# Performance work log

Measured on AMD Instinct MI355X. Metric: run time of the kernel, lower is better.

The kernel has to match this reference:

```python
import jax, jax.numpy as jnp
import numpy as np

N, E, D, R = 50000, 800000, 128, 16
NUM_OBJS, NUM_ATTRS, L = 179, 10, 5
OBJ_DIM, ATTR_DIM, HID, NANGLE = 96, 32, 512, 24


def setup_inputs() -> dict:
    key = jax.random.key(0)
    ks = jax.random.split(key, 20)
    z = jax.random.normal(ks[0], (N, D), dtype=jnp.float32)
    objs = jax.random.randint(ks[1], (N,), 0, NUM_OBJS + 1)
    s = jax.random.randint(ks[2], (E,), 0, N)
    o = jax.random.randint(ks[3], (E,), 0, N)
    p = jax.random.randint(ks[4], (E,), 0, R)
    triples = jnp.stack([s, p, o], axis=1)
    attributes = jax.random.randint(ks[5], (N,), 0, NUM_ATTRS)
    w = 0.05
    obj_emb = jax.random.normal(ks[6], (NUM_OBJS + 1, OBJ_DIM), dtype=jnp.float32)
    attr_emb = jax.random.normal(ks[7], (NUM_ATTRS, ATTR_DIM), dtype=jnp.float32)
    Wrel = jax.random.normal(ks[8], (L, R, D, D), dtype=jnp.float32) * w
    Wroot = jax.random.normal(ks[9], (L, D, D), dtype=jnp.float32) * w
    bconv = jnp.zeros((L, D), dtype=jnp.float32)
    box_W1 = jax.random.normal(ks[10], (2 * D + ATTR_DIM, HID), dtype=jnp.float32) * w
    box_b1 = jnp.zeros((HID,), dtype=jnp.float32)
    box_W2 = jax.random.normal(ks[11], (HID, 6), dtype=jnp.float32) * w
    box_b2 = jnp.zeros((6,), dtype=jnp.float32)
    ang_W1 = jax.random.normal(ks[12], (2 * D, HID), dtype=jnp.float32) * w
    ang_b1 = jnp.zeros((HID,), dtype=jnp.float32)
    ang_W2 = jax.random.normal(ks[13], (HID, NANGLE), dtype=jnp.float32) * w
    ang_b2 = jnp.zeros((NANGLE,), dtype=jnp.float32)
    return dict(z=z, objs=objs, triples=triples, attributes=attributes,
                obj_emb=obj_emb, attr_emb=attr_emb, Wrel=Wrel, Wroot=Wroot,
                bconv=bconv, box_W1=box_W1, box_b1=box_b1, box_W2=box_W2,
                box_b2=box_b2, ang_W1=ang_W1, ang_b1=ang_b1, ang_W2=ang_W2,
                ang_b2=ang_b2)


def _rgcn_layer(x, s, o, p, Wr, Wroot_l, b):
    # relation-typed transform of all nodes: [N, R, D]
    h_rel = jnp.einsum('nd,rdf->nrf', x, Wr)
    msgs = h_rel[s, p]                                   # [E, D] gather
    # mean aggregation per (target, relation), as in PyG RGCNConv
    seg = o * R + p
    cnt = jax.ops.segment_sum(jnp.ones((s.shape[0],), x.dtype), seg,
                              num_segments=x.shape[0] * R)
    deg = jnp.maximum(cnt[seg], 1.0)
    agg = jax.ops.segment_sum(msgs / deg[:, None], o, num_segments=x.shape[0])
    return x @ Wroot_l + agg + b


def reference(z, objs, triples, attributes, obj_emb, attr_emb, Wrel, Wroot,
              bconv, box_W1, box_b1, box_W2, box_b2, ang_W1, ang_b1,
              ang_W2, ang_b2):
    s, p, o = triples[:, 0], triples[:, 1], triples[:, 2]
    attr_vecs = attr_emb[attributes]                     # [N, 32]
    obj_vecs = jnp.concatenate([obj_emb[objs], attr_vecs], axis=1)  # [N, 128]
    for j in range(L):
        obj_vecs = jax.nn.relu(_rgcn_layer(obj_vecs, s, o, p,
                                           Wrel[j], Wroot[j], bconv[j]))
    obj_vecs = jnp.concatenate([obj_vecs, z], axis=1)    # [N, 256]
    obj_vecs_box = jnp.concatenate([obj_vecs, attr_vecs], axis=1)  # [N, 288]
    boxes_pred = jax.nn.relu(obj_vecs_box @ box_W1 + box_b1) @ box_W2 + box_b2
    ang_h = jax.nn.relu(obj_vecs @ ang_W1 + ang_b1) @ ang_W2 + ang_b2
    angles_pred = jax.nn.log_softmax(ang_h, axis=1)
    return boxes_pred, angles_pred
```

## Files before the change

### kernel.cpp

```cpp
#include <hip/hip_runtime.h>
#include <hip/hip_bf16.h>
#include <math.h>

#define NN   50000
#define EE   800000
#define RREL 16
#define LLAY 5
#define NBINS (NN * RREL)
#define HCAP 565248

typedef __attribute__((ext_vector_type(8))) short s8v;
typedef __attribute__((ext_vector_type(4))) float f4v;

__device__ __forceinline__ unsigned short f2bf(float f) {
  __hip_bfloat16 h = __float2bfloat16(f);
  return __builtin_bit_cast(unsigned short, h);
}
__device__ __forceinline__ float bf2f(unsigned int u) {
  return __builtin_bit_cast(float, u << 16);
}
__device__ __forceinline__ void split1(float v, unsigned short& h, unsigned short& l) {
  __hip_bfloat16 hb = __float2bfloat16(v);
  float hf = __bfloat162float(hb);
  h = __builtin_bit_cast(unsigned short, hb);
  __hip_bfloat16 lb = __float2bfloat16(v - hf);
  l = __builtin_bit_cast(unsigned short, lb);
}

__global__ void build_x0_kernel(const int* __restrict__ objs, const int* __restrict__ attrs,
                                const float* __restrict__ obj_emb, const float* __restrict__ attr_emb,
                                unsigned short* __restrict__ xh) {
  int t = blockIdx.x * blockDim.x + threadIdx.x;
  if (t >= NN * 32) return;
  int n = t >> 5, q = t & 31;
  float4 v;
  if (q < 24) v = *(const float4*)&obj_emb[(size_t)objs[n] * 96 + q * 4];
  else        v = *(const float4*)&attr_emb[(size_t)attrs[n] * 32 + (q - 24) * 4];
  ushort4 h;
  h.x = f2bf(v.x); h.y = f2bf(v.y); h.z = f2bf(v.z); h.w = f2bf(v.w);
  *(ushort4*)&xh[(size_t)n * 128 + q * 4] = h;
}

__global__ void prep_zattr(const float* __restrict__ z, const int* __restrict__ attrs,
                           const float* __restrict__ attr_emb,
                           unsigned short* __restrict__ zh, unsigned short* __restrict__ ah) {
  int t = blockIdx.x * blockDim.x + threadIdx.x;
  if (t >= NN * 40) return;
  int n = t / 40, q = t % 40;
  float4 v;
  ushort4 h;
  if (q < 32) {
    v = *(const float4*)&z[(size_t)n * 128 + q * 4];
    h.x = f2bf(v.x); h.y = f2bf(v.y); h.z = f2bf(v.z); h.w = f2bf(v.w);
    *(ushort4*)&zh[(size_t)n * 128 + q * 4] = h;
  } else {
    int qq = q - 32;
    v = *(const float4*)&attr_emb[(size_t)attrs[n] * 32 + qq * 4];
    h.x = f2bf(v.x); h.y = f2bf(v.y); h.z = f2bf(v.z); h.w = f2bf(v.w);
    *(ushort4*)&ah[(size_t)n * 32 + qq * 4] = h;
  }
}

__global__ void count_kernel(const int* __restrict__ triples, int* __restrict__ cnt) {
  int e = blockIdx.x * 256 + threadIdx.x;
  if (e >= EE) return;
  int p = triples[e * 3 + 1], o = triples[e * 3 + 2];
  atomicAdd(&cnt[o * RREL + p], 1);
}
__global__ void scanA(const int* __restrict__ cnt, int* __restrict__ binStart,
                      int* __restrict__ partial) {
  __shared__ int buf[1024];
  int g = blockIdx.x * 1024 + threadIdx.x;
  int v = (g < NBINS) ? cnt[g] : 0;
  buf[threadIdx.x] = v;
  __syncthreads();
  for (int d = 1; d < 1024; d <<= 1) {
    int t = (threadIdx.x >= d) ? buf[threadIdx.x - d] : 0;
    __syncthreads();
    buf[threadIdx.x] += t;
    __syncthreads();
  }
  if (g < NBINS) binStart[g] = buf[threadIdx.x] - v;
  if (threadIdx.x == 1023) partial[blockIdx.x] = buf[1023];
}
__global__ void scanB(int* __restrict__ partial, int* __restrict__ binStart, int nPart) {
  __shared__ int buf[1024];
  int v = (threadIdx.x < nPart) ? partial[threadIdx.x] : 0;
  buf[threadIdx.x] = v;
  __syncthreads();
  for (int d = 1; d < 1024; d <<= 1) {
    int t = (threadIdx.x >= d) ? buf[threadIdx.x - d] : 0;
    __syncthreads();
    buf[threadIdx.x] += t;
    __syncthreads();
  }
  if (threadIdx.x < nPart) partial[threadIdx.x] = buf[threadIdx.x] - v;
  if (threadIdx.x == 1023) binStart[NBINS] = buf[1023];
}
__global__ void scanC(int* __restrict__ binStart, const int* __restrict__ partial) {
  int g = blockIdx.x * 1024 + threadIdx.x;
  if (g < NBINS) binStart[g] += partial[blockIdx.x];
}

__global__ void mark_cells(const int* __restrict__ triples, int* __restrict__ sMark) {
  int e = blockIdx.x * 256 + threadIdx.x;
  if (e >= EE) return;
  int s = triples[e * 3 + 0], p = triples[e * 3 + 1];
  atomicAdd(&sMark[s * RREL + p], 1);
}
__global__ void count_dp(const int* __restrict__ sMark, int* __restrict__ Dp) {
  __shared__ int lh[RREL];
  if (threadIdx.x < RREL) lh[threadIdx.x] = 0;
  __syncthreads();
  int c = blockIdx.x * 256 + threadIdx.x;
  if (c < NBINS && sMark[c] > 0) atomicAdd(&lh[c & 15], 1);
  __syncthreads();
  if (threadIdx.x < RREL && lh[threadIdx.x] > 0)
    atomicAdd(&Dp[threadIdx.x], lh[threadIdx.x]);
}
__global__ void pad_scan(const int* __restrict__ Dp, int* __restrict__ pStart) {
  if (threadIdx.x == 0 && blockIdx.x == 0) {
    int s = 0;
    for (int p = 0; p < RREL; ++p) {
      pStart[p] = s;
      s += ((Dp[p] + 127) >> 7) << 7;
    }
    pStart[RREL] = s;
    s += ((NN + 127) >> 7) << 7;
    pStart[RREL + 1] = s;
  }
}
__global__ void assign_cells(int* __restrict__ sMark, const int* __restrict__ pStart,
                             int* __restrict__ pcur, int* __restrict__ spRel) {
  __shared__ int lh[RREL], lbase[RREL];
  if (threadIdx.x < RREL) lh[threadIdx.x] = 0;
  __syncthreads();
  int c = blockIdx.x * 256 + threadIdx.x;
  bool occ = (c < NBINS) && (sMark[c] > 0);
  int p = 0, my = 0;
  if (occ) { p = c & 15; my = atomicAdd(&lh[p], 1); }
  __syncthreads();
  if (threadIdx.x < RREL)
    lbase[threadIdx.x] = (lh[threadIdx.x] > 0)
                           ? atomicAdd(&pcur[threadIdx.x], lh[threadIdx.x]) : 0;
  __syncthreads();
  if (occ) {
    int cid = pStart[p] + lbase[p] + my;
    if (cid < HCAP) spRel[cid] = (c >> 4) * 32 + p;
    sMark[c] = cid + 1;
  }
}
__global__ void fill_root(const int* __restrict__ pStart, int* __restrict__ spRel) {
  int n = blockIdx.x * 256 + threadIdx.x;
  if (n >= NN) return;
  int cid = pStart[RREL] + n;
  if (cid < HCAP) spRel[cid] = n * 32 + 16;
}
__global__ void place_kernel(const int* __restrict__ triples, const int* __restrict__ cnt,
                             const int* __restrict__ binStart, int* __restrict__ cursor,
                             const int* __restrict__ sMark,
                             int* __restrict__ offD, float* __restrict__ wD) {
  int e = blockIdx.x * 256 + threadIdx.x;
  if (e >= EE) return;
  int s = triples[e * 3 + 0], p = triples[e * 3 + 1], o = triples[e * 3 + 2];
  int bin = o * RREL + p;
  int pos = binStart[bin] + atomicAdd(&cursor[bin], 1);
  int cid = sMark[s * RREL + p] - 1;
  offD[pos] = cid * 128;
  wD[pos] = 1.0f / (float)cnt[bin];
}

__global__ void prep_wrel(const float* __restrict__ Wrel, unsigned short* __restrict__ WT) {
  int t = blockIdx.x * 256 + threadIdx.x;
  if (t >= LLAY * RREL * 128 * 128) return;
  int f = t & 127, k = (t >> 7) & 127, lr = t >> 14;
  float v = Wrel[((size_t)lr * 128 + k) * 128 + f];
  WT[((size_t)lr * 128 + f) * 128 + k] = f2bf(v);
}
__global__ void prep_wroot(const float* __restrict__ Wroot, unsigned short* __restrict__ WT) {
  int t = blockIdx.x * 256 + threadIdx.x;
  if (t >= LLAY * 128 * 128) return;
  int f = t & 127, k = (t >> 7) & 127, l = t >> 14;
  float v = Wroot[((size_t)l * 128 + k) * 128 + f];
  WT[((size_t)l * 128 + f) * 128 + k] = f2bf(v);
}
__global__ void prep_wcat(const float* __restrict__ box_W1, const float* __restrict__ ang_W1,
                          unsigned short* __restrict__ WT) {
  int t = blockIdx.x * 256 + threadIdx.x;
  if (t >= 1024 * 288) return;
  int k = t % 288, c = t / 288;
  float v;
  if (c < 512) v = box_W1[(size_t)k * 512 + c];
  else         v = (k < 256) ? ang_W1[(size_t)k * 512 + (c - 512)] : 0.f;
  WT[(size_t)c * 288 + k] = f2bf(v);
}
__global__ void prep_bcat(const float* __restrict__ box_b1, const float* __restrict__ ang_b1,
                          float* __restrict__ bcat) {
  int t = blockIdx.x * 256 + threadIdx.x;
  if (t >= 1024) return;
  bcat[t] = (t < 512) ? box_b1[t] : ang_b1[t - 512];
}
__global__ void prep_w2cat(const float* __restrict__ box_W2, const float* __restrict__ ang_W2,
                           unsigned short* __restrict__ hi, unsigned short* __restrict__ lo) {
  int t = blockIdx.x * 256 + threadIdx.x;
  if (t >= 32 * 1024) return;
  int k = t & 1023, c = t >> 10;
  float v = 0.f;
  if (c < 6)       { if (k < 512)  v = box_W2[(size_t)k * 6 + c]; }
  else if (c < 30) { if (k >= 512) v = ang_W2[(size_t)(k - 512) * 24 + (c - 6)]; }
  split1(v, hi[(size_t)c * 1024 + k], lo[(size_t)c * 1024 + k]);
}

__global__ __launch_bounds__(256) void hrelc_mfma(const unsigned short* __restrict__ xh,
                                                  const int* __restrict__ spRel,
                                                  const unsigned short* __restrict__ Wt,
                                                  const unsigned short* __restrict__ Rt,
                                                  const float* __restrict__ bias,
                                                  const int* __restrict__ pStart,
                                                  unsigned short* __restrict__ Hc,
                                                  unsigned short* __restrict__ xr) {
  __shared__ __align__(16) unsigned short As[128][40];
  __shared__ __align__(16) unsigned short Bs[128][40];
  const int tid = threadIdx.x;
  const int row0 = blockIdx.x * 128;
  const int sr0 = spRel[row0];
  if (sr0 < 0) return;
  const int p = sr0 & 31;
  const bool isRoot = (p == 16);
  const unsigned short* WHp = isRoot ? Rt : Wt + (size_t)p * 128 * 128;

  const int wid = tid >> 6, lane = tid & 63;
  const int rg = wid >> 1, cg = wid & 1;
  const int lr = lane & 15, lk = (lane >> 4) * 8;
  f4v acc[4][4] = {};

  const int ar = tid >> 1, ahalf = tid & 1;
  const int aspv = spRel[row0 + ar];
  const int arow = (aspv >= 0) ? (aspv >> 5) : -1;
  s8v aR0, aR1;
  s8v bR[2];

  auto loadStep = [&](int k0) {
    if (arow >= 0) {
      aR0 = *(const s8v*)&xh[(size_t)arow * 128 + k0 + ahalf * 16];
      aR1 = *(const s8v*)&xh[(size_t)arow * 128 + k0 + ahalf * 16 + 8];
    } else {
      s8v zz = {0,0,0,0,0,0,0,0}; aR0 = zz; aR1 = zz;
    }
#pragma unroll
    for (int i = 0; i < 2; ++i) {
      int idx = tid + i * 256;
      int c = idx >> 2, c8 = (idx & 3) * 8;
      bR[i] = *(const s8v*)&WHp[(size_t)c * 128 + k0 + c8];
    }
  };
  auto writeStep = [&]() {
    *(s8v*)&As[ar][ahalf * 16]     = aR0;
    *(s8v*)&As[ar][ahalf * 16 + 8] = aR1;
#pragma unroll
    for (int i = 0; i < 2; ++i) {
      int idx = tid + i * 256;
      int c = idx >> 2, c8 = (idx & 3) * 8;
      *(s8v*)&Bs[c][c8] = bR[i];
    }
  };

  loadStep(0);
  for (int k0 = 0; k0 < 128; k0 += 32) {
    __syncthreads();
    writeStep();
    __syncthreads();
    if (k0 < 96) loadStep(k0 + 32);

    s8v ah[4];
#pragma unroll
    for (int mf = 0; mf < 4; ++mf) ah[mf] = *(s8v*)&As[rg * 64 + mf * 16 + lr][lk];
#pragma unroll
    for (int nf = 0; nf < 4; ++nf) {
      s8v bh_ = *(s8v*)&Bs[cg * 64 + nf * 16 + lr][lk];
#pragma unroll
      for (int mf = 0; mf < 4; ++mf) {
        acc[mf][nf] = __builtin_amdgcn_mfma_f32_16x16x32_bf16(ah[mf], bh_, acc[mf][nf], 0, 0, 0);
      }
    }
  }

  if (!isRoot) {
#pragma unroll
    for (int mf = 0; mf < 4; ++mf)
#pragma unroll
      for (int nf = 0; nf < 4; ++nf) {
        f4v v = acc[mf][nf];
        int rbase = row0 + rg * 64 + mf * 16 + (lane >> 4) * 4;
        int col = cg * 64 + nf * 16 + lr;
#pragma unroll
        for (int q = 0; q < 4; ++q)
          Hc[(size_t)(rbase + q) * 128 + col] = f2bf(v[q]);
      }
  } else {
    const int rootBase = pStart[RREL];
#pragma unroll
    for (int mf = 0; mf < 4; ++mf)
#pragma unroll
      for (int nf = 0; nf < 4; ++nf) {
        f4v v = acc[mf][nf];
        int rbase = row0 + rg * 64 + mf * 16 + (lane >> 4) * 4;
        int col = cg * 64 + nf * 16 + lr;
        float b = bias[col];
#pragma unroll
        for (int q = 0; q < 4; ++q) {
          int node = rbase + q - rootBase;
          if (node >= 0 && node < NN)
            xr[(size_t)node * 128 + col] = f2bf(v[q] + b);
        }
      }
  }
}

__global__ __launch_bounds__(256) void mlpcat_mfma(const unsigned short* __restrict__ xh,
                                                   const unsigned short* __restrict__ zh,
                                                   const unsigned short* __restrict__ ath,
                                                   const unsigned short* __restrict__ Wt,
                                                   const float* __restrict__ bcat,
                                                   unsigned short* __restrict__ H) {
  __shared__ __align__(16) unsigned short As[64][40];
  __shared__ __align__(16) unsigned short Bs[256][40];
  const int tid = threadIdx.x;
  const int row0 = blockIdx.y * 64;
  const int cb = blockIdx.x;
  const int wid = tid >> 6, lane = tid & 63;
  const int wcol = wid * 64;
  const int lr = lane & 15, lk = (lane >> 4) * 8;
  f4v acc[4][4] = {};

  s8v aR;
  s8v bR[4];
  const int ar = tid >> 2, ac8 = (tid & 3) * 8;
  const int an = row0 + ar;

  auto loadStep = [&](int k0) {
    if (an < NN) {
      if (k0 < 128)      aR = *(const s8v*)&xh[(size_t)an * 128 + k0 + ac8];
      else if (k0 < 256) aR = *(const s8v*)&zh[(size_t)an * 128 + (k0 - 128) + ac8];
      else               aR = *(const s8v*)&ath[(size_t)an * 32 + (k0 - 256) + ac8];
    } else { s8v zz = {0, 0, 0, 0, 0, 0, 0, 0}; aR = zz; }
#pragma unroll
    for (int i = 0; i < 4; ++i) {
      int idx = tid + i * 256;
      int c = idx >> 2, c8 = (idx & 3) * 8;
      int gc = cb * 256 + c;
      bR[i] = *(const s8v*)&Wt[(size_t)gc * 288 + k0 + c8];
    }
  };
  auto writeStep = [&]() {
    *(s8v*)&As[ar][ac8] = aR;
#pragma unroll
    for (int i = 0; i < 4; ++i) {
      int idx = tid + i * 256;
      int c = idx >> 2, c8 = (idx & 3) * 8;
      *(s8v*)&Bs[c][c8] = bR[i];
    }
  };

  loadStep(0);
  for (int step = 0; step < 9; ++step) {
    __syncthreads();
    writeStep();
    __syncthreads();
    if (step < 8) loadStep((step + 1) * 32);

    s8v ah[4];
#pragma unroll
    for (int mf = 0; mf < 4; ++mf) ah[mf] = *(s8v*)&As[mf * 16 + lr][lk];
#pragma unroll
    for (int nf = 0; nf < 4; ++nf) {
      s8v bh_ = *(s8v*)&Bs[wcol + nf * 16 + lr][lk];
#pragma unroll
      for (int mf = 0; mf < 4; ++mf) {
        acc[mf][nf] = __builtin_amdgcn_mfma_f32_16x16x32_bf16(ah[mf], bh_, acc[mf][nf], 0, 0, 0);
      }
    }
  }
#pragma unroll
  for (int mf = 0; mf < 4; ++mf)
#pragma unroll
    for (int nf = 0; nf < 4; ++nf) {
      int gc = cb * 256 + wcol + nf * 16 + lr;
      float b = bcat[gc];
      int rbase = row0 + mf * 16 + (lane >> 4) * 4;
#pragma unroll
      for (int q = 0; q < 4; ++q) {
        int rr = rbase + q;
        if (rr < NN) H[(size_t)rr * 1024 + gc] = f2bf(fmaxf(acc[mf][nf][q] + b, 0.f));
      }
    }
}

__global__ __launch_bounds__(256) void head_mfma(const unsigned short* __restrict__ H,
                                                 const unsigned short* __restrict__ Wh,
                                                 const unsigned short* __restrict__ Wl,
                                                 float* __restrict__ logits) {
  __shared__ __align__(16) unsigned short As[256][40];
  __shared__ __align__(16) unsigned short Bs[2][32][40];
  const int tid = threadIdx.x;
  const int row0 = blockIdx.x * 256;
  const int wid = tid >> 6, lane = tid & 63;
  const int wrow = wid * 64;
  const int lr = lane & 15, lk = (lane >> 4) * 8;
  f4v acc[4][2] = {};

  s8v aR[4];
  s8v bR;
  const int br_hl = tid >> 7, br_rem = tid & 127;
  const int br_col = br_rem >> 2, br_c8 = (br_rem & 3) * 8;

  auto loadStep = [&](int k0) {
#pragma unroll
    for (int i = 0; i < 4; ++i) {
      int idx = tid + i * 256;
      int r = idx >> 2, c8 = (idx & 3) * 8;
      int n = row0 + r;
      if (n < NN) aR[i] = *(const s8v*)&H[(size_t)n * 1024 + k0 + c8];
      else { s8v zz = {0, 0, 0, 0, 0, 0, 0, 0}; aR[i] = zz; }
    }
    const unsigned short* Wp = br_hl ? Wl : Wh;
    bR = *(const s8v*)&Wp[(size_t)br_col * 1024 + k0 + br_c8];
  };
  auto writeStep = [&]() {
#pragma unroll
    for (int i = 0; i < 4; ++i) {
      int idx = tid + i * 256;
      int r = idx >> 2, c8 = (idx & 3) * 8;
      *(s8v*)&As[r][c8] = aR[i];
    }
    *(s8v*)&Bs[br_hl][br_col][br_c8] = bR;
  };

  loadStep(0);
  for (int step = 0; step < 32; ++step) {
    __syncthreads();
    writeStep();
    __syncthreads();
    if (step < 31) loadStep((step + 1) * 32);
#pragma unroll
    for (int nf = 0; nf < 2; ++nf) {
      s8v bh_ = *(s8v*)&Bs[0][nf * 16 + lr][lk];
      s8v bl_ = *(s8v*)&Bs[1][nf * 16 + lr][lk];
#pragma unroll
      for (int mf = 0; mf < 4; ++mf) {
        s8v a_ = *(s8v*)&As[wrow + mf * 16 + lr][lk];
        acc[mf][nf] = __builtin_amdgcn_mfma_f32_16x16x32_bf16(a_, bh_, acc[mf][nf], 0, 0, 0);
        acc[mf][nf] = __builtin_amdgcn_mfma_f32_16x16x32_bf16(a_, bl_, acc[mf][nf], 0, 0, 0);
      }
    }
  }
#pragma unroll
  for (int mf = 0; mf < 4; ++mf)
#pragma unroll
    for (int nf = 0; nf < 2; ++nf) {
      int col = nf * 16 + lr;
      int rbase = row0 + wrow + mf * 16 + (lane >> 4) * 4;
#pragma unroll
      for (int q = 0; q < 4; ++q) {
        int rr = rbase + q;
        if (rr < NN) logits[(size_t)rr * 32 + col] = acc[mf][nf][q];
      }
    }
}

__global__ void head_post(const float* __restrict__ logits, const float* __restrict__ box_b2,
                          const float* __restrict__ ang_b2, float* __restrict__ out) {
  int n = blockIdx.x * 256 + threadIdx.x;
  if (n >= NN) return;
  float l[32];
#pragma unroll
  for (int i = 0; i < 8; ++i)
    *(float4*)&l[i * 4] = *(const float4*)&logits[(size_t)n * 32 + i * 4];
  float* ob = out + (size_t)n * 6;
#pragma unroll
  for (int c = 0; c < 6; ++c) ob[c] = l[c] + box_b2[c];
  float a[24];
  float mx = -1e30f;
#pragma unroll
  for (int c = 0; c < 24; ++c) { a[c] = l[6 + c] + ang_b2[c]; mx = fmaxf(mx, a[c]); }
  float ssum = 0.f;
#pragma unroll
  for (int c = 0; c < 24; ++c) ssum += expf(a[c] - mx);
  float lse = mx + logf(ssum);
  float* oa = out + (size_t)NN * 6 + (size_t)n * 24;
#pragma unroll
  for (int c = 0; c < 24; ++c) oa[c] = a[c] - lse;
}

__global__ __launch_bounds__(256) void gather_kernel(const unsigned short* __restrict__ Hc,
                                                     const int* __restrict__ binStart,
                                                     const int* __restrict__ offD,
                                                     const float* __restrict__ wD,
                                                     const unsigned short* __restrict__ xr,
                                                     unsigned short* __restrict__ xh) {
  int wid = threadIdx.x >> 6, lane = threadIdx.x & 63;
  int o = blockIdx.x * 4 + wid;
  if (o >= NN) return;
  int beg = binStart[o * RREL];
  int end = binStart[o * RREL + RREL];
  float a0 = 0.f, a1 = 0.f, b0 = 0.f, b1 = 0.f;
  float c0 = 0.f, c1 = 0.f, d0 = 0.f, d1 = 0.f;
  int i = beg;
  for (; i + 3 < end; i += 4) {
    int of1 = offD[i], of2 = offD[i + 1], of3 = offD[i + 2], of4 = offD[i + 3];
    float w1 = wD[i], w2 = wD[i + 1], w3 = wD[i + 2], w4 = wD[i + 3];
    unsigned int u1 = *(const unsigned int*)&Hc[of1 + lane * 2];
    unsigned int u2 = *(const unsigned int*)&Hc[of2 + lane * 2];
    unsigned int u3 = *(const unsigned int*)&Hc[of3 + lane * 2];
    unsigned int u4 = *(const unsigned int*)&Hc[of4 + lane * 2];
    a0 += w1 * bf2f(u1 & 0xffffu);
    a1 += w1 * bf2f(u1 >> 16);
    b0 += w2 * bf2f(u2 & 0xffffu);
    b1 += w2 * bf2f(u2 >> 16);
    c0 += w3 * bf2f(u3 & 0xffffu);
    c1 += w3 * bf2f(u3 >> 16);
    d0 += w4 * bf2f(u4 & 0xffffu);
    d1 += w4 * bf2f(u4 >> 16);
  }
  for (; i < end; ++i) {
    int of1 = offD[i];
    float w1 = wD[i];
    unsigned int u1 = *(const unsigned int*)&Hc[of1 + lane * 2];
    a0 += w1 * bf2f(u1 & 0xffffu);
    a1 += w1 * bf2f(u1 >> 16);
  }
  a0 += b0 + c0 + d0;
  a1 += b1 + c1 + d1;
  unsigned int ur = *(const unsigned int*)&xr[(size_t)o * 128 + lane * 2];
  float r0 = bf2f(ur & 0xffffu) + a0;
  float r1 = bf2f(ur >> 16) + a1;
  r0 = fmaxf(r0, 0.f); r1 = fmaxf(r1, 0.f);
  unsigned int pk = (unsigned int)f2bf(r0) | ((unsigned int)f2bf(r1) << 16);
  *(unsigned int*)&xh[(size_t)o * 128 + lane * 2] = pk;
}

extern "C" void kernel_launch(void* const* d_in, const int* in_sizes, int n_in,
                              void* d_out, int out_size, void* d_ws, size_t ws_size,
                              hipStream_t stream) {
  const float* z        = (const float*)d_in[0];
  const int*   objs     = (const int*)d_in[1];
  const int*   triples  = (const int*)d_in[2];
  const int*   attrs    = (const int*)d_in[3];
  const float* obj_emb  = (const float*)d_in[4];
  const float* attr_emb = (const float*)d_in[5];
  const float* Wrel     = (const float*)d_in[6];
  const float* Wroot    = (const float*)d_in[7];
  const float* bconv    = (const float*)d_in[8];
  const float* box_W1   = (const float*)d_in[9];
  const float* box_b1   = (const float*)d_in[10];
  const float* box_W2   = (const float*)d_in[11];
  const float* box_b2   = (const float*)d_in[12];
  const float* ang_W1   = (const float*)d_in[13];
  const float* ang_b1   = (const float*)d_in[14];
  const float* ang_W2   = (const float*)d_in[15];
  const float* ang_b2   = (const float*)d_in[16];
  float* out = (float*)d_out;

  char* base = (char*)d_ws;
  size_t cur = 0;
  auto alloc = [&](size_t bytes) -> char* {
    char* p = base + cur;
    cur += (bytes + 255) & ~(size_t)255;
    return p;
  };
  unsigned short* Hc   = (unsigned short*)alloc((size_t)HCAP * 128 * 2);
  unsigned short* xr   = (unsigned short*)alloc((size_t)NN * 128 * 2);
  unsigned short* xhi  = (unsigned short*)alloc((size_t)NN * 128 * 2);
  unsigned short* zhi  = (unsigned short*)alloc((size_t)NN * 128 * 2);
  unsigned short* athi = (unsigned short*)alloc((size_t)NN * 32 * 2);
  unsigned short* WThi = (unsigned short*)alloc((size_t)LLAY * RREL * 128 * 128 * 2);
  unsigned short* WrtH = (unsigned short*)alloc((size_t)LLAY * 128 * 128 * 2);
  unsigned short* WcH  = (unsigned short*)alloc((size_t)1024 * 288 * 2);
  unsigned short* W2H  = (unsigned short*)alloc((size_t)32 * 1024 * 2);
  unsigned short* W2L  = (unsigned short*)alloc((size_t)32 * 1024 * 2);
  float* bcat          = (float*)alloc(1024 * 4);
  float* logits        = (float*)alloc((size_t)NN * 32 * 4);
  int*   cnt      = (int*)alloc((size_t)NBINS * 4);
  int*   binStart = (int*)alloc((size_t)(NBINS + 1) * 4);
  int*   cursor   = (int*)alloc((size_t)NBINS * 4);
  int*   sMark    = (int*)alloc((size_t)NBINS * 4);
  int*   spRel    = (int*)alloc((size_t)HCAP * 4);
  int*   partial  = (int*)alloc(4096);
  int*   meta     = (int*)alloc(256);
  int*   offD     = (int*)alloc((size_t)EE * 4);
  float* wD       = (float*)alloc((size_t)EE * 4);
  int* Dp = meta, *pStart = meta + 16, *pcur = meta + 40;
  unsigned short* Hmlp = Hc;

  hipMemsetAsync(cnt, 0, (size_t)NBINS * 4, stream);
  hipMemsetAsync(cursor, 0, (size_t)NBINS * 4, stream);
  hipMemsetAsync(sMark, 0, (size_t)NBINS * 4, stream);
  hipMemsetAsync(meta, 0, 256, stream);
  hipMemsetAsync(spRel, 0xFF, (size_t)HCAP * 4, stream);

  build_x0_kernel<<<(NN * 32 + 255) / 256, 256, 0, stream>>>(objs, attrs, obj_emb, attr_emb, xhi);
  prep_zattr<<<(NN * 40 + 255) / 256, 256, 0, stream>>>(z, attrs, attr_emb, zhi, athi);
  count_kernel<<<(EE + 255) / 256, 256, 0, stream>>>(triples, cnt);
  const int nPart = (NBINS + 1023) / 1024;
  scanA<<<nPart, 1024, 0, stream>>>(cnt, binStart, partial);
  scanB<<<1, 1024, 0, stream>>>(partial, binStart, nPart);
  scanC<<<nPart, 1024, 0, stream>>>(binStart, partial);
  mark_cells<<<(EE + 255) / 256, 256, 0, stream>>>(triples, sMark);
  count_dp<<<(NBINS + 255) / 256, 256, 0, stream>>>(sMark, Dp);
  pad_scan<<<1, 64, 0, stream>>>(Dp, pStart);
  assign_cells<<<(NBINS + 255) / 256, 256, 0, stream>>>(sMark, pStart, pcur, spRel);
  fill_root<<<(NN + 255) / 256, 256, 0, stream>>>(pStart, spRel);
  place_kernel<<<(EE + 255) / 256, 256, 0, stream>>>(triples, cnt, binStart, cursor, sMark,
                                                     offD, wD);
  prep_wrel<<<(LLAY * RREL * 128 * 128 + 255) / 256, 256, 0, stream>>>(Wrel, WThi);
  prep_wroot<<<(LLAY * 128 * 128 + 255) / 256, 256, 0, stream>>>(Wroot, WrtH);
  prep_wcat<<<(1024 * 288 + 255) / 256, 256, 0, stream>>>(box_W1, ang_W1, WcH);
  prep_bcat<<<4, 256, 0, stream>>>(box_b1, ang_b1, bcat);
  prep_w2cat<<<(32 * 1024 + 255) / 256, 256, 0, stream>>>(box_W2, ang_W2, W2H, W2L);

  const int rowBlocks = (NN + 63) / 64;
  for (int j = 0; j < LLAY; ++j) {
    hrelc_mfma<<<HCAP / 128, 256, 0, stream>>>(xhi, spRel,
                                               WThi + (size_t)j * RREL * 128 * 128,
                                               WrtH + (size_t)j * 128 * 128,
                                               bconv + (size_t)j * 128, pStart, Hc, xr);
    gather_kernel<<<(NN + 3) / 4, 256, 0, stream>>>(Hc, binStart, offD, wD, xr, xhi);
  }

  mlpcat_mfma<<<dim3(4, rowBlocks), 256, 0, stream>>>(xhi, zhi, athi, WcH, bcat, Hmlp);
  head_mfma<<<(NN + 255) / 256, 256, 0, stream>>>(Hmlp, W2H, W2L, logits);
  head_post<<<(NN + 255) / 256, 256, 0, stream>>>(logits, box_b2, ang_b2, out);
}
```

Measured before the change: 864.4 us.

## Fuse second MLP layer into first-layer GEMM epilogue with split-K partial logits

The hidden activation H (N x 1024 bf16) is no longer written to global memory. Each mlpcat block now applies its 256-column slice of hidden units directly against W2 hi/lo, reducing across waves through shared memory. The four column-block partial logits are written to a partial buffer, and head_post sums them. This removes the head_mfma kernel and the round trip of H (about 100 MB written and read), at the cost of serialized per-wave epilogue work, uncoalesced W2 global loads, and 4x larger logit partials.

```diff
diff --git a/kernel.cpp b/kernel.cpp
--- a/kernel.cpp
+++ b/kernel.cpp
@@ -322,9 +322,14 @@
                                                    const unsigned short* __restrict__ ath,
                                                    const unsigned short* __restrict__ Wt,
                                                    const float* __restrict__ bcat,
-                                                   unsigned short* __restrict__ H) {
-  __shared__ __align__(16) unsigned short As[64][40];
-  __shared__ __align__(16) unsigned short Bs[256][40];
+                                                   const unsigned short* __restrict__ W2H,
+                                                   const unsigned short* __restrict__ W2L,
+                                                   float* __restrict__ logitsPart) {
+  __shared__ __align__(16) char smem[25600];
+  auto As = (unsigned short(*)[40])smem;
+  auto Bs = (unsigned short(*)[40])(smem + 5120);
+  auto ht = (unsigned short(*)[80])smem;
+  auto red = (float(*)[33])(smem + 10240);
   const int tid = threadIdx.x;
   const int row0 = blockIdx.y * 64;
   const int cb = blockIdx.x;
@@ -381,101 +386,89 @@
       }
     }
   }
+
 #pragma unroll
   for (int mf = 0; mf < 4; ++mf)
 #pragma unroll
     for (int nf = 0; nf < 4; ++nf) {
       int gc = cb * 256 + wcol + nf * 16 + lr;
       float b = bcat[gc];
-      int rbase = row0 + mf * 16 + (lane >> 4) * 4;
-#pragma unroll
-      for (int q = 0; q < 4; ++q) {
-        int rr = rbase + q;
-        if (rr < NN) H[(size_t)rr * 1024 + gc] = f2bf(fmaxf(acc[mf][nf][q] + b, 0.f));
+#pragma unroll
+      for (int q = 0; q < 4; ++q)
+        acc[mf][nf][q] = fmaxf(acc[mf][nf][q] + b, 0.f);
+    }
+
+  for (int w = 0; w < 4; ++w) {
+    __syncthreads();
+    if (wid == w) {
+#pragma unroll
+      for (int mf = 0; mf < 4; ++mf)
+#pragma unroll
+        for (int nf = 0; nf < 4; ++nf)
+#pragma unroll
+          for (int q = 0; q < 4; ++q)
+            ht[mf * 16 + (lane >> 4) * 4 + q][nf * 16 + lr] = f2bf(acc[mf][nf][q]);
+
+      f4v acc2[4][2] = {};
+#pragma unroll
+      for (int ks = 0; ks < 2; ++ks) {
+        s8v a_[4];
+#pragma unroll
+        for (int mfp = 0; mfp < 4; ++mfp)
+          a_[mfp] = *(s8v*)&ht[mfp * 16 + lr][ks * 32 + lk];
+#pragma unroll
+        for (int nfp = 0; nfp < 2; ++nfp) {
+          int kg = cb * 256 + wcol + ks * 32 + lk;
+          int n = nfp * 16 + lr;
+          s8v bh_ = *(const s8v*)&W2H[(size_t)n * 1024 + kg];
+          s8v bl_ = *(const s8v*)&W2L[(size_t)n * 1024 + kg];
+#pragma unroll
+          for (int mfp = 0; mfp < 4; ++mfp) {
+            acc2[mfp][nfp] = __builtin_amdgcn_mfma_f32_16x16x32_bf16(a_[mfp], bh_, acc2[mfp][nfp], 0, 0, 0);
+            acc2[mfp][nfp] = __builtin_amdgcn_mfma_f32_16x16x32_bf16(a_[mfp], bl_, acc2[mfp][nfp], 0, 0, 0);
+          }
+        }
       }
-    }
-}
-
-__global__ __launch_bounds__(256) void head_mfma(const unsigned short* __restrict__ H,
-                                                 const unsigned short* __restrict__ Wh,
-                                                 const unsigned short* __restrict__ Wl,
-                                                 float* __restrict__ logits) {
-  __shared__ __align__(16) unsigned short As[256][40];
-  __shared__ __align__(16) unsigned short Bs[2][32][40];
-  const int tid = threadIdx.x;
-  const int row0 = blockIdx.x * 256;
-  const int wid = tid >> 6, lane = tid & 63;
-  const int wrow = wid * 64;
-  const int lr = lane & 15, lk = (lane >> 4) * 8;
-  f4v acc[4][2] = {};
-
-  s8v aR[4];
-  s8v bR;
-  const int br_hl = tid >> 7, br_rem = tid & 127;
-  const int br_col = br_rem >> 2, br_c8 = (br_rem & 3) * 8;
-
-  auto loadStep = [&](int k0) {
-#pragma unroll
-    for (int i = 0; i < 4; ++i) {
-      int idx = tid + i * 256;
-      int r = idx >> 2, c8 = (idx & 3) * 8;
-      int n = row0 + r;
-      if (n < NN) aR[i] = *(const s8v*)&H[(size_t)n * 1024 + k0 + c8];
-      else { s8v zz = {0, 0, 0, 0, 0, 0, 0, 0}; aR[i] = zz; }
-    }
-    const unsigned short* Wp = br_hl ? Wl : Wh;
-    bR = *(const s8v*)&Wp[(size_t)br_col * 1024 + k0 + br_c8];
-  };
-  auto writeStep = [&]() {
-#pragma unroll
-    for (int i = 0; i < 4; ++i) {
-      int idx = tid + i * 256;
-      int r = idx >> 2, c8 = (idx & 3) * 8;
-      *(s8v*)&As[r][c8] = aR[i];
-    }
-    *(s8v*)&Bs[br_hl][br_col][br_c8] = bR;
-  };
-
-  loadStep(0);
-  for (int step = 0; step < 32; ++step) {
-    __syncthreads();
-    writeStep();
-    __syncthreads();
-    if (step < 31) loadStep((step + 1) * 32);
-#pragma unroll
-    for (int nf = 0; nf < 2; ++nf) {
-      s8v bh_ = *(s8v*)&Bs[0][nf * 16 + lr][lk];
-      s8v bl_ = *(s8v*)&Bs[1][nf * 16 + lr][lk];
-#pragma unroll
-      for (int mf = 0; mf < 4; ++mf) {
-        s8v a_ = *(s8v*)&As[wrow + mf * 16 + lr][lk];
-        acc[mf][nf] = __builtin_amdgcn_mfma_f32_16x16x32_bf16(a_, bh_, acc[mf][nf], 0, 0, 0);
-        acc[mf][nf] = __builtin_amdgcn_mfma_f32_16x16x32_bf16(a_, bl_, acc[mf][nf], 0, 0, 0);
-      }
-    }
-  }
-#pragma unroll
-  for (int mf = 0; mf < 4; ++mf)
-#pragma unroll
-    for (int nf = 0; nf < 2; ++nf) {
-      int col = nf * 16 + lr;
-      int rbase = row0 + wrow + mf * 16 + (lane >> 4) * 4;
-#pragma unroll
-      for (int q = 0; q < 4; ++q) {
-        int rr = rbase + q;
-        if (rr < NN) logits[(size_t)rr * 32 + col] = acc[mf][nf][q];
-      }
-    }
-}
-
-__global__ void head_post(const float* __restrict__ logits, const float* __restrict__ box_b2,
+#pragma unroll
+      for (int mfp = 0; mfp < 4; ++mfp)
+#pragma unroll
+        for (int nfp = 0; nfp < 2; ++nfp)
+#pragma unroll
+          for (int q = 0; q < 4; ++q) {
+            int node = mfp * 16 + (lane >> 4) * 4 + q;
+            int L = nfp * 16 + lr;
+            if (w == 0) red[node][L] = acc2[mfp][nfp][q];
+            else        red[node][L] += acc2[mfp][nfp][q];
+          }
+    }
+  }
+  __syncthreads();
+#pragma unroll
+  for (int i = 0; i < 8; ++i) {
+    int t = tid * 8 + i;
+    int node = t >> 5, L = t & 31;
+    int rr = row0 + node;
+    if (rr < NN) logitsPart[((size_t)cb * NN + rr) * 32 + L] = red[node][L];
+  }
+}
+
+__global__ void head_post(const float* __restrict__ logitsPart, const float* __restrict__ box_b2,
                           const float* __restrict__ ang_b2, float* __restrict__ out) {
   int n = blockIdx.x * 256 + threadIdx.x;
   if (n >= NN) return;
   float l[32];
 #pragma unroll
   for (int i = 0; i < 8; ++i)
-    *(float4*)&l[i * 4] = *(const float4*)&logits[(size_t)n * 32 + i * 4];
+    *(float4*)&l[i * 4] = *(const float4*)&logitsPart[(size_t)n * 32 + i * 4];
+#pragma unroll
+  for (int cb = 1; cb < 4; ++cb) {
+#pragma unroll
+    for (int i = 0; i < 8; ++i) {
+      float4 v = *(const float4*)&logitsPart[((size_t)cb * NN + n) * 32 + i * 4];
+      l[i * 4 + 0] += v.x; l[i * 4 + 1] += v.y;
+      l[i * 4 + 2] += v.z; l[i * 4 + 3] += v.w;
+    }
+  }
   float* ob = out + (size_t)n * 6;
 #pragma unroll
   for (int c = 0; c < 6; ++c) ob[c] = l[c] + box_b2[c];
@@ -579,7 +572,7 @@
   unsigned short* W2H  = (unsigned short*)alloc((size_t)32 * 1024 * 2);
   unsigned short* W2L  = (unsigned short*)alloc((size_t)32 * 1024 * 2);
   float* bcat          = (float*)alloc(1024 * 4);
-  float* logits        = (float*)alloc((size_t)NN * 32 * 4);
+  float* logitsPart    = (float*)alloc((size_t)4 * NN * 32 * 4);
   int*   cnt      = (int*)alloc((size_t)NBINS * 4);
   int*   binStart = (int*)alloc((size_t)(NBINS + 1) * 4);
   int*   cursor   = (int*)alloc((size_t)NBINS * 4);
@@ -590,7 +583,6 @@
   int*   offD     = (int*)alloc((size_t)EE * 4);
   float* wD       = (float*)alloc((size_t)EE * 4);
   int* Dp = meta, *pStart = meta + 16, *pcur = meta + 40;
-  unsigned short* Hmlp = Hc;
 
   hipMemsetAsync(cnt, 0, (size_t)NBINS * 4, stream);
   hipMemsetAsync(cursor, 0, (size_t)NBINS * 4, stream);
@@ -627,7 +619,7 @@
     gather_kernel<<<(NN + 3) / 4, 256, 0, stream>>>(Hc, binStart, offD, wD, xr, xhi);
   }
 
-  mlpcat_mfma<<<dim3(4, rowBlocks), 256, 0, stream>>>(xhi, zhi, athi, WcH, bcat, Hmlp);
-  head_mfma<<<(NN + 255) / 256, 256, 0, stream>>>(Hmlp, W2H, W2L, logits);
-  head_post<<<(NN + 255) / 256, 256, 0, stream>>>(logits, box_b2, ang_b2, out);
-}
+  mlpcat_mfma<<<dim3(4, rowBlocks), 256, 0, stream>>>(xhi, zhi, athi, WcH, bcat,
+                                                      W2H, W2L, logitsPart);
+  head_post<<<(NN + 255) / 256, 256, 0, stream>>>(logitsPart, box_b2, ang_b2, out);
+}
```

Result: no change. 852.3 us (-1.4%).
